# Kernel tuning notes

Measured on AMD Instinct MI355X. Metric: run time of the kernel, lower is better.

The kernel has to match this reference:

```python
import jax, jax.numpy as jnp
import numpy as np

NUM_CODES = 4096
EMBED_DIM = 64
BETA = 0.25


def setup_inputs() -> dict:
    key = jax.random.key(0)
    k1, k2 = jax.random.split(key)
    z = jax.random.normal(k1, (8, EMBED_DIM, 64, 64), dtype=jnp.float32)
    weight = jax.random.normal(k2, (NUM_CODES, EMBED_DIM), dtype=jnp.float32)
    return {"z": z, "weight": weight}


def reference(z, weight):
    # z: [B, C, H, W] -> [B, H, W, C]
    z_bhwc = jnp.moveaxis(z, 1, -1)
    z_flat = z_bhwc.reshape(-1, EMBED_DIM)  # [N, d]

    # squared-euclidean distances: ||z||^2 + ||w||^2 - 2 z.w  -> [N, num_codes]
    distance = (
        jnp.sum(z_flat ** 2, axis=1, keepdims=True)
        + jnp.sum(weight ** 2, axis=1)
        - 2.0 * jnp.einsum('bd,nd->bn', z_flat, weight)
    )
    encoding_indices = jnp.argmin(distance, axis=1)  # [N]

    # codebook lookup (gather)
    z_q = weight[encoding_indices].reshape(z_bhwc.shape)  # [B, H, W, C]

    encodings = jax.nn.one_hot(encoding_indices, NUM_CODES, dtype=z.dtype)  # [N, num_codes]
    avg_probs = jnp.mean(encodings, axis=0)
    tiny = 1e-10  # max(1e-10, finfo(fp32).tiny)
    perplexity = jnp.exp(-jnp.sum(avg_probs * jnp.log(avg_probs + tiny)))

    # commitment loss (z_q detached) — eval path, no EMA state update
    loss = BETA * jnp.mean((jax.lax.stop_gradient(z_q) - z_bhwc) ** 2)

    # straight-through estimator
    z_q = z_bhwc + jax.lax.stop_gradient(z_q - z_bhwc)
    z_q = jnp.moveaxis(z_q, -1, 1)  # back to [B, C, H, W]

    return z_q, loss, perplexity, encodings, encoding_indices
```

## Files before the change

kernel.cpp:

```cpp
#include <hip/hip_runtime.h>
#include <math.h>
#include <float.h>

#define ZQ_OFF   0
#define LOSS_OFF 2097152
#define PERP_OFF 2097153
#define ENC_OFF  2097154
#define IDX_OFF  136314882ULL
#define BETA     0.25f


typedef __attribute__((ext_vector_type(8))) short short8;
typedef __attribute__((ext_vector_type(4))) float f32x4;
typedef __attribute__((ext_vector_type(2))) float f32x2;

#define MFMA16(a, b, c) __builtin_amdgcn_mfma_f32_16x16x32_bf16(a, b, c, 0, 0, 0)

__device__ __forceinline__ float bf16_rn(float v, unsigned short* h) {
    unsigned u = __float_as_uint(v);
    unsigned r = (u + 0x7fffu + ((u >> 16) & 1u)) & 0xffff0000u;
    *h = (unsigned short)(r >> 16);
    return __uint_as_float(r);
}
__device__ __forceinline__ void split3(float v, unsigned short* h, unsigned short* m, unsigned short* l) {
    float hf = bf16_rn(v, h);
    float r1 = v - hf;
    float mf = bf16_rn(r1, m);
    float r2 = r1 - mf;
    bf16_rn(r2, l);
}

__global__ void vq_wnorm(const float* __restrict__ w, float* __restrict__ wnorm) {
    int c = blockIdx.x * 256 + threadIdx.x;
    const float4* w4 = (const float4*)(w + ((size_t)c << 6));
    float s = 0.f;
    #pragma unroll
    for (int k = 0; k < 16; ++k) { float4 v = w4[k]; s += v.x*v.x + v.y*v.y + v.z*v.z + v.w*v.w; }
    wnorm[c] = s;
}

__global__ void vq_prep(const float* __restrict__ w, unsigned short* __restrict__ w3) {
    int u = blockIdx.x * 256 + threadIdx.x;
    int c = u >> 5, slot = u & 31;
    if (slot >= 24) return;
    int p = slot >> 3, g = slot & 7;
    float4 v0 = *(const float4*)(w + ((size_t)c << 6) + g * 8);
    float4 v1 = *(const float4*)(w + ((size_t)c << 6) + g * 8 + 4);
    float vv[8] = {v0.x, v0.y, v0.z, v0.w, v1.x, v1.y, v1.z, v1.w};
    short8 o;
    #pragma unroll
    for (int e = 0; e < 8; ++e) {
        unsigned short h, m, l;
        split3(vv[e], &h, &m, &l);
        o[e] = (short)((p == 0) ? h : (p == 1) ? m : l);
    }
    char* dst = (char*)w3 + (size_t)c * 384 + (((unsigned)slot * 16) ^ (((unsigned)c & 7) << 4));
    *(short8*)dst = o;
}

__global__ __launch_bounds__(256, 2) void vq_main(
    const float* __restrict__ z, const float* __restrict__ w,
    const float* __restrict__ wnorm, const unsigned short* __restrict__ w3,
    float* __restrict__ out,
    float* __restrict__ loss_ws, int* __restrict__ ticket, int* __restrict__ hist)
{
    __shared__ __align__(16) char wl[2 * 24576];
    __shared__ float snorm[4096];
    __shared__ int s_widx[64];
    __shared__ int s_flag;

    const int tx    = threadIdx.x;
    const int lane  = tx & 63;
    const int wv    = tx >> 6;
    const int rh    = wv & 1;
    const int chalf = wv >> 1;
    const int lcol  = lane & 15;
    const int lkq   = lane >> 4;
    const int base  = blockIdx.x * 64;
    const int bb    = base >> 12;
    const int hh    = (base & 4095) >> 6;

    const char* w3b = (const char*)w3;

    {
        const char* s0 = w3b + wv * 6144 + (size_t)lane * 16;
        char* d0 = wl + wv * 6144;
        #pragma unroll
        for (int i = 0; i < 6; ++i)
            __builtin_amdgcn_global_load_lds(
                (const __attribute__((address_space(1))) void*)(s0 + i * 1024),
                (__attribute__((address_space(3))) void*)(d0 + i * 1024), 16, 0, 0);
    }

    float (*zS)[64] = (float (*)[64])(wl + 24576);
    #pragma unroll
    for (int j = 0; j < 4; ++j) {
        int f4 = j * 256 + tx;
        int d  = f4 >> 4, w4i = f4 & 15;
        float4 v = *(const float4*)(z + (((size_t)bb * 64 + d) * 64 + hh) * 64 + w4i * 4);
        *(float4*)&zS[d][w4i * 4] = v;
    }
    #pragma unroll
    for (int j = 0; j < 4; ++j) {
        int c4 = (j * 256 + tx) * 4;
        *(float4*)&snorm[c4] = *(const float4*)(wnorm + c4);
    }
    __syncthreads();

    short8 aH[2][2], aM[2][2], aL[2][2];
    #pragma unroll
    for (int u = 0; u < 2; ++u)
        #pragma unroll
        for (int s = 0; s < 2; ++s)
            #pragma unroll
            for (int j = 0; j < 8; ++j) {
                float v = zS[s * 32 + lkq * 8 + j][rh * 32 + u * 16 + lcol];
                unsigned short h, m, l;
                split3(v, &h, &m, &l);
                aH[u][s][j] = (short)h; aM[u][s][j] = (short)m; aL[u][s][j] = (short)l;
            }
    __builtin_amdgcn_sched_barrier(0);
    __builtin_amdgcn_s_barrier();
    __builtin_amdgcn_sched_barrier(0);

    float best[2][4]; int bidx[2][4];
    #pragma unroll
    for (int u = 0; u < 2; ++u)
        #pragma unroll
        for (int r = 0; r < 4; ++r) { best[u][r] = FLT_MAX; bidx[u][r] = 0; }

    float* enc = out + ENC_OFF;
    const unsigned sw = ((unsigned)lcol & 7) << 4;
    const f32x2 zero2 = {0.f, 0.f};

    #pragma unroll 1
    for (int ch = 0; ch < 64; ++ch) {
        const char* cur = wl + (ch & 1) * 24576;
        char*       nxt = wl + (~ch & 1) * 24576;

        {
            const char* s0 = w3b + (size_t)((ch + 1) & 63) * 24576 + wv * 6144 + (size_t)lane * 16;
            char* d0 = nxt + wv * 6144;
            #pragma unroll
            for (int i = 0; i < 6; ++i)
                __builtin_amdgcn_global_load_lds(
                    (const __attribute__((address_space(1))) void*)(s0 + i * 1024),
                    (__attribute__((address_space(3))) void*)(d0 + i * 1024), 16, 0, 0);
        }
        {
            f32x2* rowp = (f32x2*)(enc + ((size_t)(base + ch) << 12));
            #pragma unroll
            for (int j = 0; j < 8; ++j) {
                int slot = (wv * 512 + j * 64 + lane + 7) & 2047;
                __builtin_nontemporal_store(zero2, rowp + slot);
            }
        }
        __builtin_amdgcn_sched_barrier(0);
        asm volatile("s_waitcnt vmcnt(14)" ::: "memory");
        __builtin_amdgcn_s_barrier();
        __builtin_amdgcn_sched_barrier(0);

        {
            const int cbase = ch << 6;
            #pragma unroll
            for (int t = 0; t < 2; ++t) {
                const int clocal = chalf * 32 + t * 16 + lcol;
                const char* rowp = cur + clocal * 384;
                short8 bH0 = *(const short8*)(rowp + ((lkq * 16      ) ^ sw));
                short8 bH1 = *(const short8*)(rowp + ((lkq * 16 +  64) ^ sw));
                short8 bM0 = *(const short8*)(rowp + ((lkq * 16 + 128) ^ sw));
                short8 bM1 = *(const short8*)(rowp + ((lkq * 16 + 192) ^ sw));
                short8 bL0 = *(const short8*)(rowp + ((lkq * 16 + 256) ^ sw));
                short8 bL1 = *(const short8*)(rowp + ((lkq * 16 + 320) ^ sw));
                const float wnv = snorm[cbase + clocal];
                #pragma unroll
                for (int u = 0; u < 2; ++u) {
                    f32x4 c0 = {0.f,0.f,0.f,0.f}, c1 = {0.f,0.f,0.f,0.f}, c2 = {0.f,0.f,0.f,0.f};
                    c0 = MFMA16(aH[u][0], bH0, c0); c0 = MFMA16(aH[u][1], bH1, c0);
                    c1 = MFMA16(aH[u][0], bM0, c1); c1 = MFMA16(aH[u][1], bM1, c1);
                    c1 = MFMA16(aM[u][0], bH0, c1); c1 = MFMA16(aM[u][1], bH1, c1);
                    c2 = MFMA16(aM[u][0], bM0, c2); c2 = MFMA16(aM[u][1], bM1, c2);
                    c2 = MFMA16(aH[u][0], bL0, c2); c2 = MFMA16(aH[u][1], bL1, c2);
                    c2 = MFMA16(aL[u][0], bH0, c2); c2 = MFMA16(aL[u][1], bH1, c2);
                    #pragma unroll
                    for (int r = 0; r < 4; ++r) {
                        float sdot = (c0[r] + c1[r]) + c2[r];
                        float dd = fmaf(-2.f, sdot, wnv);
                        if (dd < best[u][r]) { best[u][r] = dd; bidx[u][r] = cbase + clocal; }
                    }
                }
            }
        }
        __builtin_amdgcn_sched_barrier(0);
        __builtin_amdgcn_s_barrier();
    }

    __syncthreads();

    #pragma unroll
    for (int u = 0; u < 2; ++u)
        #pragma unroll
        for (int mm = 1; mm < 16; mm <<= 1)
            #pragma unroll
            for (int r = 0; r < 4; ++r) {
                float ob = __shfl_xor(best[u][r], mm, 64);
                int   oi = __shfl_xor(bidx[u][r], mm, 64);
                if (ob < best[u][r] || (ob == best[u][r] && oi < bidx[u][r])) {
                    best[u][r] = ob; bidx[u][r] = oi;
                }
            }

    float2* s_red = (float2*)snorm;
    if (lcol == 0) {
        #pragma unroll
        for (int u = 0; u < 2; ++u)
            #pragma unroll
            for (int r = 0; r < 4; ++r) {
                int row = rh * 32 + u * 16 + lkq * 4 + r;
                s_red[row * 2 + chalf] = make_float2(best[u][r], __int_as_float(bidx[u][r]));
            }
    }
    __syncthreads();

    if (tx < 64) {
        float2 a = s_red[tx * 2], b2 = s_red[tx * 2 + 1];
        int ai = __float_as_int(a.y), bi2 = __float_as_int(b2.y);
        int bi; float bv;
        if (a.x < b2.x || (a.x == b2.x && ai < bi2)) { bv = a.x; bi = ai; }
        else                                          { bv = b2.x; bi = bi2; }
        (void)bv;
        s_widx[tx] = bi;
        __builtin_nontemporal_store((float)bi, out + IDX_OFF + (size_t)(base + tx));
        atomicAdd(&hist[bi], 1);
        __builtin_nontemporal_store(1.0f, enc + ((size_t)(base + tx) << 12) + bi);
    }
    __syncthreads();

    {
        const int row = tx & 63;
        const int dg  = tx >> 6;
        const int wi  = s_widx[row];
        const float* qrow = w + ((size_t)wi << 6);
        float lsum = 0.f;
        #pragma unroll
        for (int dd = 0; dd < 16; ++dd) {
            int d = dg * 16 + dd;
            float qv = qrow[d];
            float zv = z[(((size_t)bb * 64 + d) * 64 + hh) * 64 + row];
            float diff = qv - zv;
            lsum += diff * diff;
            __builtin_nontemporal_store(zv + (qv - zv),
                out + ZQ_OFF + (((size_t)bb * 64 + d) * 64 + hh) * 64 + row);
        }
        #pragma unroll
        for (int off = 32; off > 0; off >>= 1) lsum += __shfl_down(lsum, off, 64);
        if ((tx & 63) == 0) atomicAdd(loss_ws, lsum);
    }

    __syncthreads();
    if (tx == 0) {
        __threadfence();
        int old = atomicAdd(ticket, 1);
        s_flag = (old == 511) ? 1 : 0;
    }
    __syncthreads();
    if (s_flag) {
        __threadfence();
        float s = 0.f;
        #pragma unroll
        for (int j = 0; j < 16; ++j) {
            int c = tx + j * 256;
            int cnt = atomicAdd(&hist[c], 0);
            float p = (float)cnt * (1.f / 32768.f);
            s += p * logf(p + 1e-10f);
        }
        float* fr = snorm;
        fr[tx] = s;
        __syncthreads();
        for (int off = 128; off > 0; off >>= 1) {
            if (tx < off) fr[tx] += fr[tx + off];
            __syncthreads();
        }
        if (tx == 0) {
            out[LOSS_OFF] = BETA * atomicAdd(loss_ws, 0.f) / 2097152.f;
            out[PERP_OFF] = expf(-fr[0]);
        }
    }
}

extern "C" void kernel_launch(void* const* d_in, const int* in_sizes, int n_in,
                              void* d_out, int out_size, void* d_ws, size_t ws_size,
                              hipStream_t stream)
{
    const float* z = (const float*)d_in[0];
    const float* w = (const float*)d_in[1];
    float* out     = (float*)d_out;
    float* loss_ws = (float*)d_ws;
    int*   ticket  = (int*)((char*)d_ws + 4);
    int*   hist    = (int*)((char*)d_ws + 16);
    float* wnorm   = (float*)((char*)d_ws + 16400);
    unsigned short* w3 = (unsigned short*)((char*)d_ws + 32800);
    (void)ws_size; (void)in_sizes; (void)n_in; (void)out_size;

    hipMemsetAsync(d_ws, 0, 16 + 4096 * sizeof(int), stream);
    vq_wnorm<<<16, 256, 0, stream>>>(w, wnorm);
    vq_prep<<<512, 256, 0, stream>>>(w, w3);
    vq_main<<<512, 256, 0, stream>>>(z, w, wnorm, w3, out, loss_ws, ticket, hist);
}
```

Before: 601.0 us.

## Give each wave a private codebook double-buffer and drop per-chunk block barriers

The codebook streaming loop now works in 32-code chunks, 128 iterations in all. Each wave loads its own 16-code slice into a private LDS double-buffer, so the two block-wide barriers per iteration are gone and waves rely only on their own vmcnt waits. This removes cross-wave stalls, so each wave's loads and MFMAs can run at its own pace. The cost is that waves sharing a code half now load the same slice twice, doubling codebook L2-to-LDS traffic. The encoding zero-fill is spread across the halved chunks, and the final one-hot store now uses a normal store instead of a nontemporal one.

```diff
diff --git a/kernel.cpp b/kernel.cpp
--- a/kernel.cpp
+++ b/kernel.cpp
@@ -64,7 +64,7 @@
     float* __restrict__ out,
     float* __restrict__ loss_ws, int* __restrict__ ticket, int* __restrict__ hist)
 {
-    __shared__ __align__(16) char wl[2 * 24576];
+    __shared__ __align__(16) char wl[2 * 4 * 6144];
     __shared__ float snorm[4096];
     __shared__ int s_widx[64];
     __shared__ int s_flag;
@@ -83,7 +83,7 @@
     const char* w3b = (const char*)w3;
 
     {
-        const char* s0 = w3b + wv * 6144 + (size_t)lane * 16;
+        const char* s0 = w3b + (size_t)(chalf * 16) * 384 + (size_t)lane * 16;
         char* d0 = wl + wv * 6144;
         #pragma unroll
         for (int i = 0; i < 6; ++i)
@@ -134,13 +134,11 @@
     const f32x2 zero2 = {0.f, 0.f};
 
     #pragma unroll 1
-    for (int ch = 0; ch < 64; ++ch) {
-        const char* cur = wl + (ch & 1) * 24576;
-        char*       nxt = wl + (~ch & 1) * 24576;
-
+    for (int ch = 0; ch < 128; ++ch) {
         {
-            const char* s0 = w3b + (size_t)((ch + 1) & 63) * 24576 + wv * 6144 + (size_t)lane * 16;
-            char* d0 = nxt + wv * 6144;
+            const char* s0 = w3b + (size_t)((((ch + 1) & 127) * 32 + chalf * 16)) * 384
+                           + (size_t)lane * 16;
+            char* d0 = wl + ((~ch & 1) * 4 + wv) * 6144;
             #pragma unroll
             for (int i = 0; i < 6; ++i)
                 __builtin_amdgcn_global_load_lds(
@@ -148,51 +146,44 @@
                     (__attribute__((address_space(3))) void*)(d0 + i * 1024), 16, 0, 0);
         }
         {
-            f32x2* rowp = (f32x2*)(enc + ((size_t)(base + ch) << 12));
-            #pragma unroll
-            for (int j = 0; j < 8; ++j) {
-                int slot = (wv * 512 + j * 64 + lane + 7) & 2047;
+            f32x2* rowp = (f32x2*)(enc + ((size_t)(base + (ch >> 1)) << 12));
+            #pragma unroll
+            for (int j = 0; j < 4; ++j) {
+                int slot = (ch & 1) * 1024 + ((j * 256 + tx + 7) & 1023);
                 __builtin_nontemporal_store(zero2, rowp + slot);
             }
         }
         __builtin_amdgcn_sched_barrier(0);
         asm volatile("s_waitcnt vmcnt(14)" ::: "memory");
-        __builtin_amdgcn_s_barrier();
         __builtin_amdgcn_sched_barrier(0);
 
         {
-            const int cbase = ch << 6;
-            #pragma unroll
-            for (int t = 0; t < 2; ++t) {
-                const int clocal = chalf * 32 + t * 16 + lcol;
-                const char* rowp = cur + clocal * 384;
-                short8 bH0 = *(const short8*)(rowp + ((lkq * 16      ) ^ sw));
-                short8 bH1 = *(const short8*)(rowp + ((lkq * 16 +  64) ^ sw));
-                short8 bM0 = *(const short8*)(rowp + ((lkq * 16 + 128) ^ sw));
-                short8 bM1 = *(const short8*)(rowp + ((lkq * 16 + 192) ^ sw));
-                short8 bL0 = *(const short8*)(rowp + ((lkq * 16 + 256) ^ sw));
-                short8 bL1 = *(const short8*)(rowp + ((lkq * 16 + 320) ^ sw));
-                const float wnv = snorm[cbase + clocal];
+            const int code0 = ch * 32 + chalf * 16;
+            const char* rowp = wl + ((ch & 1) * 4 + wv) * 6144 + lcol * 384;
+            short8 bH0 = *(const short8*)(rowp + ((lkq * 16      ) ^ sw));
+            short8 bH1 = *(const short8*)(rowp + ((lkq * 16 +  64) ^ sw));
+            short8 bM0 = *(const short8*)(rowp + ((lkq * 16 + 128) ^ sw));
+            short8 bM1 = *(const short8*)(rowp + ((lkq * 16 + 192) ^ sw));
+            short8 bL0 = *(const short8*)(rowp + ((lkq * 16 + 256) ^ sw));
+            short8 bL1 = *(const short8*)(rowp + ((lkq * 16 + 320) ^ sw));
+            const float wnv = snorm[code0 + lcol];
+            #pragma unroll
+            for (int u = 0; u < 2; ++u) {
+                f32x4 c0 = {0.f,0.f,0.f,0.f}, c1 = {0.f,0.f,0.f,0.f}, c2 = {0.f,0.f,0.f,0.f};
+                c0 = MFMA16(aH[u][0], bH0, c0); c0 = MFMA16(aH[u][1], bH1, c0);
+                c1 = MFMA16(aH[u][0], bM0, c1); c1 = MFMA16(aH[u][1], bM1, c1);
+                c1 = MFMA16(aM[u][0], bH0, c1); c1 = MFMA16(aM[u][1], bH1, c1);
+                c2 = MFMA16(aM[u][0], bM0, c2); c2 = MFMA16(aM[u][1], bM1, c2);
+                c2 = MFMA16(aH[u][0], bL0, c2); c2 = MFMA16(aH[u][1], bL1, c2);
+                c2 = MFMA16(aL[u][0], bH0, c2); c2 = MFMA16(aL[u][1], bH1, c2);
                 #pragma unroll
-                for (int u = 0; u < 2; ++u) {
-                    f32x4 c0 = {0.f,0.f,0.f,0.f}, c1 = {0.f,0.f,0.f,0.f}, c2 = {0.f,0.f,0.f,0.f};
-                    c0 = MFMA16(aH[u][0], bH0, c0); c0 = MFMA16(aH[u][1], bH1, c0);
-                    c1 = MFMA16(aH[u][0], bM0, c1); c1 = MFMA16(aH[u][1], bM1, c1);
-                    c1 = MFMA16(aM[u][0], bH0, c1); c1 = MFMA16(aM[u][1], bH1, c1);
-                    c2 = MFMA16(aM[u][0], bM0, c2); c2 = MFMA16(aM[u][1], bM1, c2);
-                    c2 = MFMA16(aH[u][0], bL0, c2); c2 = MFMA16(aH[u][1], bL1, c2);
-                    c2 = MFMA16(aL[u][0], bH0, c2); c2 = MFMA16(aL[u][1], bH1, c2);
-                    #pragma unroll
-                    for (int r = 0; r < 4; ++r) {
-                        float sdot = (c0[r] + c1[r]) + c2[r];
-                        float dd = fmaf(-2.f, sdot, wnv);
-                        if (dd < best[u][r]) { best[u][r] = dd; bidx[u][r] = cbase + clocal; }
-                    }
+                for (int r = 0; r < 4; ++r) {
+                    float sdot = (c0[r] + c1[r]) + c2[r];
+                    float dd = fmaf(-2.f, sdot, wnv);
+                    if (dd < best[u][r]) { best[u][r] = dd; bidx[u][r] = code0 + lcol; }
                 }
             }
         }
-        __builtin_amdgcn_sched_barrier(0);
-        __builtin_amdgcn_s_barrier();
     }
 
     __syncthreads();
@@ -225,14 +216,12 @@
     if (tx < 64) {
         float2 a = s_red[tx * 2], b2 = s_red[tx * 2 + 1];
         int ai = __float_as_int(a.y), bi2 = __float_as_int(b2.y);
-        int bi; float bv;
-        if (a.x < b2.x || (a.x == b2.x && ai < bi2)) { bv = a.x; bi = ai; }
-        else                                          { bv = b2.x; bi = bi2; }
-        (void)bv;
+        int bi;
+        if (a.x < b2.x || (a.x == b2.x && ai < bi2)) bi = ai; else bi = bi2;
         s_widx[tx] = bi;
         __builtin_nontemporal_store((float)bi, out + IDX_OFF + (size_t)(base + tx));
         atomicAdd(&hist[bi], 1);
-        __builtin_nontemporal_store(1.0f, enc + ((size_t)(base + tx) << 12) + bi);
+        enc[((size_t)(base + tx) << 12) + bi] = 1.0f;
     }
     __syncthreads();
 
```

New measurement: 609.7 us. About the same (+1.4%).

## Process 128 rows per block to double codebook reuse per LDS tile

Applied to the files above, without the earlier changes.

Each block now handles 128 input vectors instead of 64, so every codebook chunk staged in LDS feeds twice as many MFMA rows and global codebook traffic per row halves. The grid shrinks to 256 blocks at one block per CU, and the z tile is kept in a dedicated shared buffer so the epilogue reads z from LDS instead of re-reading global memory. The cost is more registers for the A fragments and running best values, lower occupancy, and fewer blocks than CUs on the device, which may leave compute units idle.

```diff
diff --git a/kernel.cpp b/kernel.cpp
--- a/kernel.cpp
+++ b/kernel.cpp
@@ -58,27 +58,28 @@
     *(short8*)dst = o;
 }
 
-__global__ __launch_bounds__(256, 2) void vq_main(
+__global__ __launch_bounds__(256, 1) void vq_main(
     const float* __restrict__ z, const float* __restrict__ w,
     const float* __restrict__ wnorm, const unsigned short* __restrict__ w3,
     float* __restrict__ out,
     float* __restrict__ loss_ws, int* __restrict__ ticket, int* __restrict__ hist)
 {
     __shared__ __align__(16) char wl[2 * 24576];
+    __shared__ float zS[64][128];
     __shared__ float snorm[4096];
-    __shared__ int s_widx[64];
+    __shared__ int s_widx[128];
     __shared__ int s_flag;
 
     const int tx    = threadIdx.x;
     const int lane  = tx & 63;
     const int wv    = tx >> 6;
-    const int rh    = wv & 1;
+    const int rg    = wv & 1;
     const int chalf = wv >> 1;
     const int lcol  = lane & 15;
     const int lkq   = lane >> 4;
-    const int base  = blockIdx.x * 64;
+    const int base  = blockIdx.x * 128;
     const int bb    = base >> 12;
-    const int hh    = (base & 4095) >> 6;
+    const int hh0   = (base & 4095) >> 6;
 
     const char* w3b = (const char*)w3;
 
@@ -92,12 +93,11 @@
                 (__attribute__((address_space(3))) void*)(d0 + i * 1024), 16, 0, 0);
     }
 
-    float (*zS)[64] = (float (*)[64])(wl + 24576);
-    #pragma unroll
-    for (int j = 0; j < 4; ++j) {
+    #pragma unroll
+    for (int j = 0; j < 8; ++j) {
         int f4 = j * 256 + tx;
-        int d  = f4 >> 4, w4i = f4 & 15;
-        float4 v = *(const float4*)(z + (((size_t)bb * 64 + d) * 64 + hh) * 64 + w4i * 4);
+        int d  = f4 >> 5, w4i = f4 & 31;
+        float4 v = *(const float4*)(z + (((size_t)bb * 64 + d) * 64 + hh0) * 64 + w4i * 4);
         *(float4*)&zS[d][w4i * 4] = v;
     }
     #pragma unroll
@@ -107,14 +107,14 @@
     }
     __syncthreads();
 
-    short8 aH[2][2], aM[2][2], aL[2][2];
-    #pragma unroll
-    for (int u = 0; u < 2; ++u)
+    short8 aH[4][2], aM[4][2], aL[4][2];
+    #pragma unroll
+    for (int u = 0; u < 4; ++u)
         #pragma unroll
         for (int s = 0; s < 2; ++s)
             #pragma unroll
             for (int j = 0; j < 8; ++j) {
-                float v = zS[s * 32 + lkq * 8 + j][rh * 32 + u * 16 + lcol];
+                float v = zS[s * 32 + lkq * 8 + j][rg * 64 + u * 16 + lcol];
                 unsigned short h, m, l;
                 split3(v, &h, &m, &l);
                 aH[u][s][j] = (short)h; aM[u][s][j] = (short)m; aL[u][s][j] = (short)l;
@@ -123,9 +123,9 @@
     __builtin_amdgcn_s_barrier();
     __builtin_amdgcn_sched_barrier(0);
 
-    float best[2][4]; int bidx[2][4];
-    #pragma unroll
-    for (int u = 0; u < 2; ++u)
+    float best[4][4]; int bidx[4][4];
+    #pragma unroll
+    for (int u = 0; u < 4; ++u)
         #pragma unroll
         for (int r = 0; r < 4; ++r) { best[u][r] = FLT_MAX; bidx[u][r] = 0; }
 
@@ -148,15 +148,15 @@
                     (__attribute__((address_space(3))) void*)(d0 + i * 1024), 16, 0, 0);
         }
         {
-            f32x2* rowp = (f32x2*)(enc + ((size_t)(base + ch) << 12));
-            #pragma unroll
-            for (int j = 0; j < 8; ++j) {
-                int slot = (wv * 512 + j * 64 + lane + 7) & 2047;
+            f32x2* rowp = (f32x2*)(enc + ((size_t)(base + ch * 2 + chalf) << 12));
+            #pragma unroll
+            for (int j = 0; j < 16; ++j) {
+                int slot = rg * 1024 + ((j * 64 + lane + 7) & 1023);
                 __builtin_nontemporal_store(zero2, rowp + slot);
             }
         }
         __builtin_amdgcn_sched_barrier(0);
-        asm volatile("s_waitcnt vmcnt(14)" ::: "memory");
+        asm volatile("s_waitcnt vmcnt(38)" ::: "memory");
         __builtin_amdgcn_s_barrier();
         __builtin_amdgcn_sched_barrier(0);
 
@@ -174,7 +174,7 @@
                 short8 bL1 = *(const short8*)(rowp + ((lkq * 16 + 320) ^ sw));
                 const float wnv = snorm[cbase + clocal];
                 #pragma unroll
-                for (int u = 0; u < 2; ++u) {
+                for (int u = 0; u < 4; ++u) {
                     f32x4 c0 = {0.f,0.f,0.f,0.f}, c1 = {0.f,0.f,0.f,0.f}, c2 = {0.f,0.f,0.f,0.f};
                     c0 = MFMA16(aH[u][0], bH0, c0); c0 = MFMA16(aH[u][1], bH1, c0);
                     c1 = MFMA16(aH[u][0], bM0, c1); c1 = MFMA16(aH[u][1], bM1, c1);
@@ -198,7 +198,7 @@
     __syncthreads();
 
     #pragma unroll
-    for (int u = 0; u < 2; ++u)
+    for (int u = 0; u < 4; ++u)
         #pragma unroll
         for (int mm = 1; mm < 16; mm <<= 1)
             #pragma unroll
@@ -213,55 +213,54 @@
     float2* s_red = (float2*)snorm;
     if (lcol == 0) {
         #pragma unroll
-        for (int u = 0; u < 2; ++u)
+        for (int u = 0; u < 4; ++u)
             #pragma unroll
             for (int r = 0; r < 4; ++r) {
-                int row = rh * 32 + u * 16 + lkq * 4 + r;
+                int row = rg * 64 + u * 16 + lkq * 4 + r;
                 s_red[row * 2 + chalf] = make_float2(best[u][r], __int_as_float(bidx[u][r]));
             }
     }
     __syncthreads();
 
-    if (tx < 64) {
+    if (tx < 128) {
         float2 a = s_red[tx * 2], b2 = s_red[tx * 2 + 1];
         int ai = __float_as_int(a.y), bi2 = __float_as_int(b2.y);
-        int bi; float bv;
-        if (a.x < b2.x || (a.x == b2.x && ai < bi2)) { bv = a.x; bi = ai; }
-        else                                          { bv = b2.x; bi = bi2; }
-        (void)bv;
+        int bi;
+        if (a.x < b2.x || (a.x == b2.x && ai < bi2)) bi = ai; else bi = bi2;
         s_widx[tx] = bi;
         __builtin_nontemporal_store((float)bi, out + IDX_OFF + (size_t)(base + tx));
         atomicAdd(&hist[bi], 1);
-        __builtin_nontemporal_store(1.0f, enc + ((size_t)(base + tx) << 12) + bi);
+        enc[((size_t)(base + tx) << 12) + bi] = 1.0f;
     }
     __syncthreads();
 
     {
-        const int row = tx & 63;
-        const int dg  = tx >> 6;
+        const int row = lane + (wv & 1) * 64;
+        const int dg  = wv >> 1;
         const int wi  = s_widx[row];
         const float* qrow = w + ((size_t)wi << 6);
+        const int hh = hh0 + (row >> 6), ww = row & 63;
         float lsum = 0.f;
         #pragma unroll
-        for (int dd = 0; dd < 16; ++dd) {
-            int d = dg * 16 + dd;
+        for (int dd = 0; dd < 32; ++dd) {
+            int d = dg * 32 + dd;
             float qv = qrow[d];
-            float zv = z[(((size_t)bb * 64 + d) * 64 + hh) * 64 + row];
+            float zv = zS[d][row];
             float diff = qv - zv;
             lsum += diff * diff;
             __builtin_nontemporal_store(zv + (qv - zv),
-                out + ZQ_OFF + (((size_t)bb * 64 + d) * 64 + hh) * 64 + row);
+                out + ZQ_OFF + (((size_t)bb * 64 + d) * 64 + hh) * 64 + ww);
         }
         #pragma unroll
         for (int off = 32; off > 0; off >>= 1) lsum += __shfl_down(lsum, off, 64);
-        if ((tx & 63) == 0) atomicAdd(loss_ws, lsum);
+        if (lane == 0) atomicAdd(loss_ws, lsum);
     }
 
     __syncthreads();
     if (tx == 0) {
         __threadfence();
         int old = atomicAdd(ticket, 1);
-        s_flag = (old == 511) ? 1 : 0;
+        s_flag = (old == 255) ? 1 : 0;
     }
     __syncthreads();
     if (s_flag) {
@@ -305,5 +304,5 @@
     hipMemsetAsync(d_ws, 0, 16 + 4096 * sizeof(int), stream);
     vq_wnorm<<<16, 256, 0, stream>>>(w, wnorm);
     vq_prep<<<512, 256, 0, stream>>>(w, w3);
-    vq_main<<<512, 256, 0, stream>>>(z, w, wnorm, w3, out, loss_ws, ticket, hist);
-}
+    vq_main<<<256, 256, 0, stream>>>(z, w, wnorm, w3, out, loss_ws, ticket, hist);
+}
```

Result: slower. 626.3 us (+4.2%).
